# Kernel optimization log

Hardware: AMD Instinct MI355X
Metric: run time of the kernel (lower is better)

## Reference

```python
import jax, jax.numpy as jnp
import numpy as np


def _pairwise_sqdist(a, b):
    # a: [B,N,2], b: [B,M,2] -> [B,N,M] squared Euclidean distances
    a2 = jnp.sum(a * a, axis=-1)  # [B,N]
    b2 = jnp.sum(b * b, axis=-1)  # [B,M]
    ab = jnp.einsum('bnd,bmd->bnm', a, b)  # [B,N,M]
    return a2[:, :, None] + b2[:, None, :] - 2.0 * ab


def setup_inputs() -> dict:
    key = jax.random.key(0)
    k1, k2 = jax.random.split(key)
    B, N, M, D = 16, 2048, 2048, 2
    preds = jax.random.normal(k1, (B, N, D), dtype=jnp.float32)
    targs = jax.random.normal(k2, (B, M, D), dtype=jnp.float32)
    subcoef = jnp.ones((D,), dtype=jnp.float32)
    return {"preds": preds, "targs": targs, "subcoef": subcoef}


def reference(preds, targs, subcoef):
    # Bidirectional Chamfer-style NN L1 loss, faithful to NNLoss.nn_loss.
    d2 = _pairwise_sqdist(preds, targs)  # [B,N,M]

    # preds -> nearest GT (KDTree over targs queried with preds)
    nn_t = jnp.argmin(d2, axis=2)  # [B,N]
    matched_t = jnp.take_along_axis(targs, nn_t[:, :, None], axis=1)  # [B,N,2]
    move_preds_to_gt = jnp.sum(jnp.abs(preds - matched_t) * subcoef)

    # targs -> nearest pred (KDTree over preds queried with targs)
    nn_p = jnp.argmin(d2, axis=1)  # [B,M]
    matched_p = jnp.take_along_axis(preds, nn_p[:, :, None], axis=1)  # [B,M,2]
    move_gts_to_pred = jnp.sum(jnp.abs(matched_p - targs))

    return move_gts_to_pred + move_preds_to_gt
```

## Files before the change

kernel.cpp:

```cpp
#include <hip/hip_runtime.h>


constexpr int B      = 16;
constexpr int NPTS   = 2048;
constexpr int BLK    = 1024;
constexpr int G      = 256;
constexpr int S      = 16;
constexpr int QPT    = 4;
constexpr int SEGLEN = NPTS / S;
constexpr int ITERS  = SEGLEN / 2;
constexpr int NBLK   = 2 * B * (NPTS / G);

__global__ __launch_bounds__(BLK) void nn_main(
    const float* __restrict__ preds, const float* __restrict__ targs,
    const float* __restrict__ subcoef, float* __restrict__ ws_out)
{
    __shared__ float4 sdb4[NPTS / 2];
    __shared__ unsigned long long cand[S][G];
    __shared__ float ssum[BLK / 64];

    const int blk  = blockIdx.x;
    const int dir  = blk >> 7;
    const int b    = (blk >> 3) & 15;
    const int tile = blk & 7;

    const float2* qb = reinterpret_cast<const float2*>(dir == 0 ? preds : targs)
                       + b * NPTS + tile * G;
    const float2* db = reinterpret_cast<const float2*>(dir == 0 ? targs : preds)
                       + b * NPTS;

    const float4* db4 = reinterpret_cast<const float4*>(db);
    for (int i = threadIdx.x; i < NPTS / 2; i += BLK) sdb4[i] = db4[i];

    const int qslot = threadIdx.x & 63;
    const int seg   = threadIdx.x >> 6;

    float m2x[QPT], m2y[QPT], best[QPT];
    int   bi[QPT];
    #pragma unroll
    for (int q = 0; q < QPT; ++q) {
        const float2 qp = qb[qslot + q * 64];
        m2x[q] = -2.0f * qp.x;
        m2y[q] = -2.0f * qp.y;
        best[q] = 3.402823466e+38f;
        bi[q] = 0;
    }
    __syncthreads();

    const int pbase   = seg * ITERS;
    const int idxBase = seg * SEGLEN;
    #pragma unroll 8
    for (int i = 0; i < ITERS; ++i) {
        const float4 p = sdb4[pbase + i];
        const float t20 = fmaf(p.x, p.x, p.y * p.y);
        const float t21 = fmaf(p.z, p.z, p.w * p.w);
        const int i0 = idxBase + 2 * i;
        #pragma unroll
        for (int q = 0; q < QPT; ++q) {
            const float d0 = fmaf(m2x[q], p.x, fmaf(m2y[q], p.y, t20));
            if (d0 < best[q]) { best[q] = d0; bi[q] = i0; }
            const float d1 = fmaf(m2x[q], p.z, fmaf(m2y[q], p.w, t21));
            if (d1 < best[q]) { best[q] = d1; bi[q] = i0 + 1; }
        }
    }

    #pragma unroll
    for (int q = 0; q < QPT; ++q) {
        unsigned int fb = __float_as_uint(best[q]);
        fb ^= 0x80000000u | (unsigned int)((int)fb >> 31);
        cand[seg][qslot + q * 64] =
            ((unsigned long long)fb << 32) | (unsigned int)bi[q];
    }
    __syncthreads();

    float val = 0.0f;
    if (threadIdx.x < G) {
        unsigned long long bp = cand[0][threadIdx.x];
        #pragma unroll
        for (int s = 1; s < S; ++s) {
            const unsigned long long v = cand[s][threadIdx.x];
            bp = v < bp ? v : bp;
        }
        const int idx = (int)(unsigned int)bp;
        const float2 qp = qb[threadIdx.x];
        const float2 tp = db[idx];
        float sx = 1.0f, sy = 1.0f;
        if (dir == 0) { sx = subcoef[0]; sy = subcoef[1]; }
        val = fabsf(qp.x - tp.x) * sx + fabsf(qp.y - tp.y) * sy;
    }

    #pragma unroll
    for (int off = 32; off > 0; off >>= 1)
        val += __shfl_down(val, off, 64);
    if ((threadIdx.x & 63) == 0) ssum[threadIdx.x >> 6] = val;
    __syncthreads();
    if (threadIdx.x == 0) {
        float s = ssum[0];
        #pragma unroll
        for (int w = 1; w < BLK / 64; ++w) s += ssum[w];
        ws_out[blk] = s;
    }
}

__global__ __launch_bounds__(NBLK) void nn_reduce(
    const float* __restrict__ ws_in, float* __restrict__ out)
{
    __shared__ float ssum[NBLK / 64];
    float val = ws_in[threadIdx.x];
    #pragma unroll
    for (int off = 32; off > 0; off >>= 1)
        val += __shfl_down(val, off, 64);
    if ((threadIdx.x & 63) == 0) ssum[threadIdx.x >> 6] = val;
    __syncthreads();
    if (threadIdx.x == 0) {
        float s = ssum[0];
        #pragma unroll
        for (int w = 1; w < NBLK / 64; ++w) s += ssum[w];
        out[0] = s;
    }
}

extern "C" void kernel_launch(void* const* d_in, const int* in_sizes, int n_in,
                              void* d_out, int out_size, void* d_ws, size_t ws_size,
                              hipStream_t stream) {
    const float* preds   = (const float*)d_in[0];
    const float* targs   = (const float*)d_in[1];
    const float* subcoef = (const float*)d_in[2];
    float* out = (float*)d_out;
    float* ws  = (float*)d_ws;

    nn_main<<<NBLK, BLK, 0, stream>>>(preds, targs, subcoef, ws);
    nn_reduce<<<1, NBLK, 0, stream>>>(ws, out);
}
```

Baseline: 76.06 us.

## Use packed FMA with SoA shared layout and more queries per thread

```diff
diff --git a/kernel.cpp b/kernel.cpp
--- a/kernel.cpp
+++ b/kernel.cpp
@@ -1,66 +1,80 @@
 #include <hip/hip_runtime.h>
 
 
+typedef float v2f __attribute__((ext_vector_type(2)));
+
 constexpr int B      = 16;
 constexpr int NPTS   = 2048;
-constexpr int BLK    = 1024;
-constexpr int G      = 256;
-constexpr int S      = 16;
-constexpr int QPT    = 4;
+constexpr int BLK    = 512;
+constexpr int G      = 128;
+constexpr int QPT    = 8;
+constexpr int QG     = G / QPT;
+constexpr int S      = BLK / QG;
 constexpr int SEGLEN = NPTS / S;
 constexpr int ITERS  = SEGLEN / 2;
+constexpr int SSTR   = SEGLEN + 4;
 constexpr int NBLK   = 2 * B * (NPTS / G);
 
-__global__ __launch_bounds__(BLK) void nn_main(
+__global__ __launch_bounds__(BLK, 4) void nn_main(
     const float* __restrict__ preds, const float* __restrict__ targs,
     const float* __restrict__ subcoef, float* __restrict__ ws_out)
 {
-    __shared__ float4 sdb4[NPTS / 2];
-    __shared__ unsigned long long cand[S][G];
+    __shared__ float sx[S * SSTR];
+    __shared__ float sy[S * SSTR];
+    __shared__ unsigned long long cand[S * G];
     __shared__ float ssum[BLK / 64];
 
     const int blk  = blockIdx.x;
-    const int dir  = blk >> 7;
-    const int b    = (blk >> 3) & 15;
-    const int tile = blk & 7;
+    const int dir  = blk >> 8;
+    const int b    = (blk >> 4) & 15;
+    const int tile = blk & 15;
 
     const float2* qb = reinterpret_cast<const float2*>(dir == 0 ? preds : targs)
                        + b * NPTS + tile * G;
     const float2* db = reinterpret_cast<const float2*>(dir == 0 ? targs : preds)
                        + b * NPTS;
 
-    const float4* db4 = reinterpret_cast<const float4*>(db);
-    for (int i = threadIdx.x; i < NPTS / 2; i += BLK) sdb4[i] = db4[i];
+    for (int i = threadIdx.x; i < NPTS; i += BLK) {
+        const float2 p = db[i];
+        const int slot = (i >> 6) * SSTR + (i & 63);
+        sx[slot] = p.x;
+        sy[slot] = p.y;
+    }
 
-    const int qslot = threadIdx.x & 63;
-    const int seg   = threadIdx.x >> 6;
+    const int qg  = threadIdx.x & (QG - 1);
+    const int seg = threadIdx.x / QG;
 
-    float m2x[QPT], m2y[QPT], best[QPT];
+    v2f   m2x[QPT], m2y[QPT];
+    float best[QPT];
     int   bi[QPT];
     #pragma unroll
     for (int q = 0; q < QPT; ++q) {
-        const float2 qp = qb[qslot + q * 64];
-        m2x[q] = -2.0f * qp.x;
-        m2y[q] = -2.0f * qp.y;
+        const float2 qp = qb[qg + q * QG];
+        const float ax = -2.0f * qp.x, ay = -2.0f * qp.y;
+        m2x[q] = {ax, ax};
+        m2y[q] = {ay, ay};
         best[q] = 3.402823466e+38f;
         bi[q] = 0;
     }
     __syncthreads();
 
-    const int pbase   = seg * ITERS;
+    const v2f* sxp = reinterpret_cast<const v2f*>(sx + seg * SSTR);
+    const v2f* syp = reinterpret_cast<const v2f*>(sy + seg * SSTR);
     const int idxBase = seg * SEGLEN;
-    #pragma unroll 8
+    #pragma unroll 4
     for (int i = 0; i < ITERS; ++i) {
-        const float4 p = sdb4[pbase + i];
-        const float t20 = fmaf(p.x, p.x, p.y * p.y);
-        const float t21 = fmaf(p.z, p.z, p.w * p.w);
+        const v2f px = sxp[i];
+        const v2f py = syp[i];
+        const v2f t2 = __builtin_elementwise_fma(px, px, py * py);
         const int i0 = idxBase + 2 * i;
         #pragma unroll
         for (int q = 0; q < QPT; ++q) {
-            const float d0 = fmaf(m2x[q], p.x, fmaf(m2y[q], p.y, t20));
-            if (d0 < best[q]) { best[q] = d0; bi[q] = i0; }
-            const float d1 = fmaf(m2x[q], p.z, fmaf(m2y[q], p.w, t21));
-            if (d1 < best[q]) { best[q] = d1; bi[q] = i0 + 1; }
+            const v2f d = __builtin_elementwise_fma(
+                m2x[q], px, __builtin_elementwise_fma(m2y[q], py, t2));
+            const bool lt = d.y < d.x;
+            const float dm = lt ? d.y : d.x;
+            const int   im = lt ? i0 + 1 : i0;
+            if (dm < best[q]) { best[q] = dm; bi[q] = im; }
         }
     }
 
@@ -68,25 +82,25 @@
     for (int q = 0; q < QPT; ++q) {
         unsigned int fb = __float_as_uint(best[q]);
         fb ^= 0x80000000u | (unsigned int)((int)fb >> 31);
-        cand[seg][qslot + q * 64] =
+        cand[seg * G + qg + q * QG] =
             ((unsigned long long)fb << 32) | (unsigned int)bi[q];
     }
     __syncthreads();
 
     float val = 0.0f;
     if (threadIdx.x < G) {
-        unsigned long long bp = cand[0][threadIdx.x];
+        unsigned long long bp = cand[threadIdx.x];
         #pragma unroll
         for (int s = 1; s < S; ++s) {
-            const unsigned long long v = cand[s][threadIdx.x];
+            const unsigned long long v = cand[s * G + threadIdx.x];
             bp = v < bp ? v : bp;
         }
         const int idx = (int)(unsigned int)bp;
         const float2 qp = qb[threadIdx.x];
         const float2 tp = db[idx];
-        float sx = 1.0f, sy = 1.0f;
-        if (dir == 0) { sx = subcoef[0]; sy = subcoef[1]; }
-        val = fabsf(qp.x - tp.x) * sx + fabsf(qp.y - tp.y) * sy;
+        float sxc = 1.0f, syc = 1.0f;
+        if (dir == 0) { sxc = subcoef[0]; syc = subcoef[1]; }
+        val = fabsf(qp.x - tp.x) * sxc + fabsf(qp.y - tp.y) * syc;
     }
 
     #pragma unroll
```

After: 77.46 us. Within noise of the previous version (+1.8%).
